# Performance work log

Hardware: AMD Instinct MI355X
Metric: run time of the kernel (lower is better)

## Reference

```python
import jax, jax.numpy as jnp
import numpy as np

NEG_SLOPE = 0.2

def gat_conv(x, edge_index, W, a_src, a_dst, b):
    # PyG GATConv, heads=1, eval mode (dropout off), add_self_loops=True
    N = x.shape[0]
    h = x @ W                                   # [N, C]
    loops = jnp.arange(N, dtype=edge_index.dtype)
    src = jnp.concatenate([edge_index[0], loops])
    dst = jnp.concatenate([edge_index[1], loops])
    s_src = h @ a_src                            # [N]
    s_dst = h @ a_dst                            # [N]
    e = s_src[src] + s_dst[dst]                  # [E+N]
    e = jnp.where(e > 0, e, NEG_SLOPE * e)       # leaky_relu
    # segment softmax over destination neighborhoods
    m = jax.ops.segment_max(e, dst, num_segments=N)
    ex = jnp.exp(e - m[dst])
    denom = jax.ops.segment_sum(ex, dst, num_segments=N)
    alpha = ex / denom[dst]                      # [E+N]
    out = jax.ops.segment_sum(alpha[:, None] * h[src], dst, num_segments=N)
    return out + b

def setup_inputs() -> dict:
    key = jax.random.key(0)
    ks = jax.random.split(key, 10)
    N, F_in, H, C, E = 100000, 256, 128, 40, 1600000
    x = jax.random.normal(ks[0], (N, F_in), dtype=jnp.float32)
    edge_index = jax.random.randint(ks[1], (2, E), 0, N, dtype=jnp.int64)
    s1 = 1.0 / np.sqrt(F_in)
    s2 = 1.0 / np.sqrt(H)
    W1 = jax.random.normal(ks[2], (F_in, H), dtype=jnp.float32) * s1
    a_src1 = jax.random.normal(ks[3], (H,), dtype=jnp.float32) * s2
    a_dst1 = jax.random.normal(ks[4], (H,), dtype=jnp.float32) * s2
    b1 = jnp.zeros((H,), dtype=jnp.float32)
    W2 = jax.random.normal(ks[5], (H, C), dtype=jnp.float32) * s2
    a_src2 = jax.random.normal(ks[6], (C,), dtype=jnp.float32) * 0.1
    a_dst2 = jax.random.normal(ks[7], (C,), dtype=jnp.float32) * 0.1
    b2 = jnp.zeros((C,), dtype=jnp.float32)
    return {"x": x, "edge_index": edge_index, "W1": W1, "a_src1": a_src1,
            "a_dst1": a_dst1, "b1": b1, "W2": W2, "a_src2": a_src2,
            "a_dst2": a_dst2, "b2": b2}

def reference(x, edge_index, W1, a_src1, a_dst1, b1, W2, a_src2, a_dst2, b2):
    h = gat_conv(x, edge_index, W1, a_src1, a_dst1, b1)
    h = jax.nn.relu(h)
    # dropout(p=0.6) is identity in eval mode
    h = gat_conv(h, edge_index, W2, a_src2, a_dst2, b2)
    return jax.nn.log_softmax(h, axis=1)
```

## Files before the change

### kernel.cpp

```cpp
#include <hip/hip_runtime.h>
#include <math.h>

#define NEG_SLOPE 0.2f
#define CAP 64
#define NB 64
#define NBUCKET 1563
#define BCAP 1408
#define BINCHUNK 2048
#define NBIN2 782

typedef __attribute__((ext_vector_type(8))) short short8;
typedef __attribute__((ext_vector_type(4))) short short4v;
typedef __attribute__((ext_vector_type(4))) float f32x4;
typedef __attribute__((ext_vector_type(2))) float f32x2;

__device__ inline unsigned short f2bf(float f) {
    union { float f; unsigned u; } x; x.f = f;
    unsigned r = x.u + 0x7FFFu + ((x.u >> 16) & 1u);
    return (unsigned short)(r >> 16);
}

__device__ __forceinline__ void gload_lds16(const void* g, void* l) {
    __builtin_amdgcn_global_load_lds(
        (const __attribute__((address_space(1))) void*)g,
        (__attribute__((address_space(3))) void*)l, 16, 0, 0);
}


__global__ __launch_bounds__(256) void front_kernel(
    const int* __restrict__ ei, int* __restrict__ bcnt,
    unsigned* __restrict__ bbuf, int E,
    const float* __restrict__ W1, const float* __restrict__ W2,
    short* __restrict__ bsw1, short* __restrict__ bsw2)
{
    __shared__ int lc[NBUCKET];
    const int tid = threadIdx.x;

    if (blockIdx.x < NBIN2) {
        const int base = blockIdx.x * BINCHUNK;
        int n = E - base; if (n > BINCHUNK) n = BINCHUNK;

        for (int b = tid; b < NBUCKET; b += 256) lc[b] = 0;
        __syncthreads();
        for (int i = tid; i < n; i += 256)
            atomicAdd(&lc[ei[E + base + i] >> 6], 1);
        __syncthreads();
        for (int b = tid; b < NBUCKET; b += 256) {
            int c = lc[b];
            lc[b] = c ? atomicAdd(&bcnt[b], c) : 0;
        }
        __syncthreads();
        for (int i = tid; i < n; i += 256) {
            int s = ei[base + i];
            int d = ei[E + base + i];
            int b = d >> 6;
            int pos = atomicAdd(&lc[b], 1);
            if (pos < BCAP)
                bbuf[(size_t)b * BCAP + pos] = (unsigned)s | ((unsigned)(d & 63) << 17);
        }
    } else {
        int t = (blockIdx.x - NBIN2) * 256 + tid;
        if (t < 4096) {
            int lane = t & 63;
            int f = t >> 6;
            int k_step = f & 7;
            int n_tile = f >> 3;
            int n  = n_tile * 16 + (lane & 15);
            int k0 = k_step * 32 + (lane >> 4) * 8;
            short8 v;
            #pragma unroll
            for (int j = 0; j < 8; j++)
                v[j] = (short)f2bf(W1[(size_t)(k0 + j) * 128 + n]);
            ((short8*)bsw1)[t] = v;
        } else if (t < 4096 + 768) {
            int u = t - 4096;
            int lane = u & 63;
            int f = u >> 6;
            int k_step = f & 3;
            int n_tile = f >> 2;
            int n  = n_tile * 16 + (lane & 15);
            int k0 = k_step * 32 + (lane >> 4) * 8;
            short8 v;
            #pragma unroll
            for (int j = 0; j < 8; j++)
                v[j] = (n < 40) ? (short)f2bf(W2[(size_t)(k0 + j) * 40 + n]) : (short)0;
            ((short8*)bsw2)[u] = v;
        }
    }
}

__global__ __launch_bounds__(256, 2) void mid_kernel(
    const int* __restrict__ bcnt, const unsigned* __restrict__ bbuf,
    int* __restrict__ csr, int* __restrict__ sorted, int* __restrict__ clsCnt,
    const float* __restrict__ x, const short* __restrict__ bsw,
    const float* __restrict__ a_src, const float* __restrict__ a_dst,
    unsigned char* __restrict__ h1, float* __restrict__ s_src,
    float* __restrict__ s_dst, int M)
{
    __shared__ __align__(16) char smem[16896];
    const int tid = threadIdx.x;
    const int bi = blockIdx.x;
    const int vb = bi >> 1;

    if ((bi & 1) == 0) {
        int* lcnt = (int*)smem;
        int (*lcsr)[CAP] = (int(*)[CAP])(smem + 256);
        int* chist = (int*)(smem + 256 + 16384);
        int* cbase = (int*)(smem + 256 + 16384 + 16);

        const int b = vb;
        const int nb = b * NB;

        if (tid < NB) lcnt[tid] = 0;
        if (tid < 4) chist[tid] = 0;
        __syncthreads();

        if (tid < NB && nb + tid < M) {
            int pos = atomicAdd(&lcnt[tid], 1);
            if (pos < CAP) lcsr[tid][pos] = nb + tid;
        }

        int ne = bcnt[b]; if (ne > BCAP) ne = BCAP;
        const unsigned* __restrict__ bp = bbuf + (size_t)b * BCAP;
        for (int j = tid; j < ne; j += 256) {
            unsigned v = bp[j];
            int s  = v & 0x1FFFF;
            int dl = v >> 17;
            int pos = atomicAdd(&lcnt[dl], 1);
            if (pos < CAP) lcsr[dl][pos] = s;
        }
        __syncthreads();

        const int4* __restrict__ srcp = (const int4*)&lcsr[0][0];
        int4* __restrict__ dstp = (int4*)(csr + (size_t)nb * CAP);
        #pragma unroll 4
        for (int j = tid; j < NB * CAP / 4; j += 256) dstp[j] = srcp[j];

        int deg = 0, cls = 0, pos = 0;
        bool isNode = (tid < NB && nb + tid < M);
        if (isNode) {
            deg = lcnt[tid]; if (deg > CAP) deg = CAP;
            cls = (deg - 1) >> 4;
            pos = atomicAdd(&chist[cls], 1);
        }
        __syncthreads();
        if (tid < 4) cbase[tid] = chist[tid] ? atomicAdd(&clsCnt[tid], chist[tid]) : 0;
        __syncthreads();
        if (isNode)
            sorted[(size_t)cls * M + cbase[cls] + pos] = (nb + tid) | (deg << 17);
        return;
    }

    const int wave = tid >> 6, lane = tid & 63;
    short8* lbs = (short8*)smem;
    const int rowBase = vb * 64;
    const int arow = rowBase + wave * 16 + (lane & 15);
    const int acol0 = (lane >> 4) * 8;
    const bool rv = (arow < M);
    const float* __restrict__ xr = x + (size_t)arow * 256 + acol0;
    const char* __restrict__ bsb = (const char*)bsw;

    auto stage = [&](int buf, int nt) {
        const char* s = bsb + nt * 8192 + wave * 2048 + lane * 16;
        char* d = smem + buf * 8192 + wave * 2048 + lane * 16;
        gload_lds16(s, d);
        gload_lds16(s + 1024, d + 1024);
    };

    stage(0, 0);

    float4 px[8], qx[8];
    #pragma unroll
    for (int k = 0; k < 8; k++) {
        px[k] = make_float4(0.f, 0.f, 0.f, 0.f);
        qx[k] = px[k];
        if (rv) {
            px[k] = *(const float4*)(xr + k * 32);
            qx[k] = *(const float4*)(xr + k * 32 + 4);
        }
    }
    short8 a[8];
    #pragma unroll
    for (int k = 0; k < 8; k++) {
        short8 t;
        t[0] = (short)f2bf(px[k].x); t[1] = (short)f2bf(px[k].y);
        t[2] = (short)f2bf(px[k].z); t[3] = (short)f2bf(px[k].w);
        t[4] = (short)f2bf(qx[k].x); t[5] = (short)f2bf(qx[k].y);
        t[6] = (short)f2bf(qx[k].z); t[7] = (short)f2bf(qx[k].w);
        a[k] = t;
    }

    const int R0 = rowBase + wave * 16 + (lane >> 4) * 4;
    const int Cb = lane & 15;

    float asv[8], adv[8];
    #pragma unroll
    for (int nt = 0; nt < 8; nt++) {
        asv[nt] = a_src[nt * 16 + Cb];
        adv[nt] = a_dst[nt * 16 + Cb];
    }

    stage(1, 1);

    float ss[4] = {0.f, 0.f, 0.f, 0.f};
    float sd[4] = {0.f, 0.f, 0.f, 0.f};
    f32x4 prev = {0.f, 0.f, 0.f, 0.f};
    int wpk[4][4];

    #pragma unroll
    for (int nt = 0; nt < 8; nt++) {
        if (nt == 7) asm volatile("s_waitcnt vmcnt(0)" ::: "memory");
        else         asm volatile("s_waitcnt vmcnt(2)" ::: "memory");
        __builtin_amdgcn_s_barrier();

        short8 breg[8];
        #pragma unroll
        for (int k = 0; k < 8; k++) breg[k] = lbs[(nt & 1) * 512 + k * 64 + lane];
        asm volatile("s_waitcnt lgkmcnt(0)" ::: "memory");
        __builtin_amdgcn_sched_barrier(0);
        __builtin_amdgcn_s_barrier();

        if (nt < 6) stage(nt & 1, nt + 2);

        __builtin_amdgcn_s_setprio(1);
        f32x4 acc = {0.f, 0.f, 0.f, 0.f};
        #pragma unroll
        for (int k = 0; k < 8; k++)
            acc = __builtin_amdgcn_mfma_f32_16x16x32_bf16(a[k], breg[k], acc, 0, 0, 0);
        __builtin_amdgcn_s_setprio(0);

        float as_ = asv[nt], ad_ = adv[nt];
        #pragma unroll
        for (int r = 0; r < 4; r++) {
            float v = acc[r];
            ss[r] = fmaf(v, as_, ss[r]);
            sd[r] = fmaf(v, ad_, sd[r]);
        }
        if (nt & 1) {
            #pragma unroll
            for (int r = 0; r < 4; r++)
                wpk[nt >> 1][r] = __builtin_amdgcn_cvt_pk_fp8_f32(prev[r], acc[r], 0, false);
        } else {
            prev = acc;
        }
    }

    #pragma unroll
    for (int r = 0; r < 4; r++) {
        int R = R0 + r;
        if (R < M) {
            #pragma unroll
            for (int t = 0; t < 4; t++)
                *(unsigned short*)(h1 + (size_t)R * 128 + t * 32 + 2 * Cb) =
                    (unsigned short)wpk[t][r];
        }
    }
    #pragma unroll
    for (int off = 1; off < 16; off <<= 1) {
        #pragma unroll
        for (int r = 0; r < 4; r++) {
            ss[r] += __shfl_xor(ss[r], off);
            sd[r] += __shfl_xor(sd[r], off);
        }
    }
    if ((lane & 15) == 0) {
        #pragma unroll
        for (int r = 0; r < 4; r++) {
            int R = R0 + r;
            if (R < M) { s_src[R] = ss[r]; s_dst[R] = sd[r]; }
        }
    }
}

__global__ __launch_bounds__(256, 4) void agg1_kernel(
    const unsigned char* __restrict__ h, const int* __restrict__ csr,
    const int* __restrict__ sorted, const int* __restrict__ clsCnt,
    const float* __restrict__ s_src, const float* __restrict__ s_dst,
    const float* __restrict__ bias,
    const short* __restrict__ bsw2,
    const float* __restrict__ a_src2, const float* __restrict__ a_dst2,
    unsigned char* __restrict__ h2, float* __restrict__ ss2,
    float* __restrict__ sd2, int N)
{
    __shared__ short lrow[16][136];
    __shared__ int   lnode[16];
    const int tid = threadIdx.x;
    const int lane = tid & 63;
    const int c = lane & 15;
    const int base = lane & 48;
    const int grp = tid >> 4;
    const int g = blockIdx.x * 16 + grp;

    int c0 = clsCnt[0], c01 = c0 + clsCnt[1], c012 = c01 + clsCnt[2];
    int cls, local;
    if (g < c0)        { cls = 0; local = g; }
    else if (g < c01)  { cls = 1; local = g - c0; }
    else if (g < c012) { cls = 2; local = g - c01; }
    else               { cls = 3; local = g - c012; }

    int ent = sorted[(size_t)cls * N + local];
    int n = ent & 0x1FFFF;
    int deg = ent >> 17;
    const int* __restrict__ edges = csr + (size_t)n * CAP;
    float sdn = s_dst[n];

    int s0 = 0, s1 = 0, s2 = 0, s3 = 0;
    float e0 = -1e30f, e1 = -1e30f, e2 = -1e30f, e3 = -1e30f;
    if (c < deg)      { s0 = edges[c];      e0 = s_src[s0] + sdn; }
    if (c + 16 < deg) { s1 = edges[c + 16]; e1 = s_src[s1] + sdn; }
    if (c + 32 < deg) { s2 = edges[c + 32]; e2 = s_src[s2] + sdn; }
    if (c + 48 < deg) { s3 = edges[c + 48]; e3 = s_src[s3] + sdn; }
    e0 = e0 > 0.f ? e0 : NEG_SLOPE * e0;
    e1 = e1 > 0.f ? e1 : NEG_SLOPE * e1;
    e2 = e2 > 0.f ? e2 : NEG_SLOPE * e2;
    e3 = e3 > 0.f ? e3 : NEG_SLOPE * e3;
    float m = fmaxf(fmaxf(e0, e1), fmaxf(e2, e3));
    #pragma unroll
    for (int off = 1; off < 16; off <<= 1) m = fmaxf(m, __shfl_xor(m, off));
    float w0 = (c < deg)      ? __expf(e0 - m) : 0.f;
    float w1 = (c + 16 < deg) ? __expf(e1 - m) : 0.f;
    float w2 = (c + 32 < deg) ? __expf(e2 - m) : 0.f;
    float w3 = (c + 48 < deg) ? __expf(e3 - m) : 0.f;
    float denom = (w0 + w1) + (w2 + w3);
    #pragma unroll
    for (int off = 1; off < 16; off <<= 1) denom += __shfl_xor(denom, off);
    float inv = 1.0f / denom;

    const uint2* __restrict__ hp = (const uint2*)h;
    f32x2 acc0 = {0.f, 0.f}, acc1 = {0.f, 0.f}, acc2 = {0.f, 0.f}, acc3 = {0.f, 0.f};

#define AGG1_BLK(K, SK, WK)                                                  \
    if (16 * K < deg) {                                                      \
        uint2 u[16];                                                         \
        _Pragma("unroll")                                                    \
        for (int jj = 0; jj < 16; jj++) {                                    \
            int sv = __shfl(SK, base + jj);                                  \
            u[jj] = hp[(size_t)sv * 16 + c];                                 \
        }                                                                    \
        _Pragma("unroll")                                                    \
        for (int jj = 0; jj < 16; jj++) {                                    \
            float wv = __shfl(WK, base + jj);                                \
            f32x2 p;                                                         \
            p = __builtin_amdgcn_cvt_pk_f32_fp8(u[jj].x, false); acc0 += p * wv; \
            p = __builtin_amdgcn_cvt_pk_f32_fp8(u[jj].x, true);  acc1 += p * wv; \
            p = __builtin_amdgcn_cvt_pk_f32_fp8(u[jj].y, false); acc2 += p * wv; \
            p = __builtin_amdgcn_cvt_pk_f32_fp8(u[jj].y, true);  acc3 += p * wv; \
        }                                                                    \
    }
    AGG1_BLK(0, s0, w0)
    AGG1_BLK(1, s1, w1)
    AGG1_BLK(2, s2, w2)
    AGG1_BLK(3, s3, w3)
#undef AGG1_BLK

    int cA = 32 * (c >> 2) + 4 * (c & 3);
    float4 bA = *(const float4*)&bias[cA];
    float4 bB = *(const float4*)&bias[cA + 16];
    float r0 = fmaxf(fmaf(acc0.x, inv, bA.x), 0.f);
    float r1 = fmaxf(fmaf(acc1.x, inv, bA.y), 0.f);
    float r2 = fmaxf(fmaf(acc2.x, inv, bA.z), 0.f);
    float r3 = fmaxf(fmaf(acc3.x, inv, bA.w), 0.f);
    float q0 = fmaxf(fmaf(acc0.y, inv, bB.x), 0.f);
    float q1 = fmaxf(fmaf(acc1.y, inv, bB.y), 0.f);
    float q2 = fmaxf(fmaf(acc2.y, inv, bB.z), 0.f);
    float q3 = fmaxf(fmaf(acc3.y, inv, bB.w), 0.f);
    short4v oA = { (short)f2bf(r0), (short)f2bf(r1), (short)f2bf(r2), (short)f2bf(r3) };
    short4v oB = { (short)f2bf(q0), (short)f2bf(q1), (short)f2bf(q2), (short)f2bf(q3) };
    *(short4v*)&lrow[grp][cA] = oA;
    *(short4v*)&lrow[grp][cA + 16] = oB;
    if (c == 0) lnode[grp] = n;
    __syncthreads();

    if (tid >= 64) return;

    const short8* __restrict__ bs = (const short8*)bsw2;
    short8 a[4];
    #pragma unroll
    for (int k = 0; k < 4; k++)
        a[k] = *(const short8*)&lrow[lane & 15][(lane >> 4) * 8 + k * 32];

    float accs[3][4];
    float ssv[4] = {0.f, 0.f, 0.f, 0.f};
    float sdv[4] = {0.f, 0.f, 0.f, 0.f};

    #pragma unroll
    for (int nt = 0; nt < 3; nt++) {
        f32x4 acc = {0.f, 0.f, 0.f, 0.f};
        #pragma unroll
        for (int k = 0; k < 4; k++) {
            short8 b = bs[(nt * 4 + k) * 64 + lane];
            acc = __builtin_amdgcn_mfma_f32_16x16x32_bf16(a[k], b, acc, 0, 0, 0);
        }
        int C = nt * 16 + c;
        bool valid = (C < 40);
        float as_ = valid ? a_src2[C] : 0.f;
        float ad_ = valid ? a_dst2[C] : 0.f;
        #pragma unroll
        for (int r = 0; r < 4; r++) {
            float v = acc[r];
            accs[nt][r] = v;
            ssv[r] = fmaf(v, as_, ssv[r]);
            sdv[r] = fmaf(v, ad_, sdv[r]);
        }
    }
    #pragma unroll
    for (int r = 0; r < 4; r++) {
        int node = lnode[(lane >> 4) * 4 + r];
        int wA = __builtin_amdgcn_cvt_pk_fp8_f32(accs[0][r], accs[1][r], 0, false);
        int wB = __builtin_amdgcn_cvt_pk_fp8_f32(accs[2][r], 0.f, 0, false);
        *(unsigned short*)(h2 + (size_t)node * 64 + 2 * c) = (unsigned short)wA;
        *(unsigned short*)(h2 + (size_t)node * 64 + 32 + 2 * c) = (unsigned short)wB;
    }
    #pragma unroll
    for (int off = 1; off < 16; off <<= 1) {
        #pragma unroll
        for (int r = 0; r < 4; r++) {
            ssv[r] += __shfl_xor(ssv[r], off);
            sdv[r] += __shfl_xor(sdv[r], off);
        }
    }
    if (c == 0) {
        #pragma unroll
        for (int r = 0; r < 4; r++) {
            int node = lnode[(lane >> 4) * 4 + r];
            ss2[node] = ssv[r];
            sd2[node] = sdv[r];
        }
    }
}

__global__ __launch_bounds__(256, 4) void agg2_kernel(
    const unsigned char* __restrict__ h, const int* __restrict__ csr,
    const int* __restrict__ sorted, const int* __restrict__ clsCnt,
    const float* __restrict__ s_src, const float* __restrict__ s_dst,
    const float* __restrict__ bias, float* __restrict__ out, int N)
{
    const int lane = threadIdx.x & 63;
    const int c = lane & 15;
    const int base = lane & 48;
    const int g = blockIdx.x * 16 + (threadIdx.x >> 4);

    int c0 = clsCnt[0], c01 = c0 + clsCnt[1], c012 = c01 + clsCnt[2];
    int cls, local;
    if (g < c0)        { cls = 0; local = g; }
    else if (g < c01)  { cls = 1; local = g - c0; }
    else if (g < c012) { cls = 2; local = g - c01; }
    else               { cls = 3; local = g - c012; }

    int ent = sorted[(size_t)cls * N + local];
    int n = ent & 0x1FFFF;
    int deg = ent >> 17;
    const int* __restrict__ edges = csr + (size_t)n * CAP;
    float sdn = s_dst[n];

    int s0 = 0, s1 = 0, s2 = 0, s3 = 0;
    float e0 = -1e30f, e1 = -1e30f, e2 = -1e30f, e3 = -1e30f;
    if (c < deg)      { s0 = edges[c];      e0 = s_src[s0] + sdn; }
    if (c + 16 < deg) { s1 = edges[c + 16]; e1 = s_src[s1] + sdn; }
    if (c + 32 < deg) { s2 = edges[c + 32]; e2 = s_src[s2] + sdn; }
    if (c + 48 < deg) { s3 = edges[c + 48]; e3 = s_src[s3] + sdn; }
    e0 = e0 > 0.f ? e0 : NEG_SLOPE * e0;
    e1 = e1 > 0.f ? e1 : NEG_SLOPE * e1;
    e2 = e2 > 0.f ? e2 : NEG_SLOPE * e2;
    e3 = e3 > 0.f ? e3 : NEG_SLOPE * e3;
    float m = fmaxf(fmaxf(e0, e1), fmaxf(e2, e3));
    #pragma unroll
    for (int off = 1; off < 16; off <<= 1) m = fmaxf(m, __shfl_xor(m, off));
    float w0 = (c < deg)      ? __expf(e0 - m) : 0.f;
    float w1 = (c + 16 < deg) ? __expf(e1 - m) : 0.f;
    float w2 = (c + 32 < deg) ? __expf(e2 - m) : 0.f;
    float w3 = (c + 48 < deg) ? __expf(e3 - m) : 0.f;
    float denom = (w0 + w1) + (w2 + w3);
    #pragma unroll
    for (int off = 1; off < 16; off <<= 1) denom += __shfl_xor(denom, off);
    float inv = 1.0f / denom;

    const unsigned* __restrict__ hp = (const unsigned*)h;
    f32x2 acc0 = {0.f, 0.f}, acc1 = {0.f, 0.f};

#define AGG2_BLK(K, SK, WK)                                                  \
    if (16 * K < deg) {                                                      \
        unsigned u[16];                                                      \
        _Pragma("unroll")                                                    \
        for (int jj = 0; jj < 16; jj++) {                                    \
            int sv = __shfl(SK, base + jj);                                  \
            u[jj] = hp[(size_t)sv * 16 + c];                                 \
        }                                                                    \
        _Pragma("unroll")                                                    \
        for (int jj = 0; jj < 16; jj++) {                                    \
            float wv = __shfl(WK, base + jj);                                \
            f32x2 p;                                                         \
            p = __builtin_amdgcn_cvt_pk_f32_fp8(u[jj], false); acc0 += p * wv; \
            p = __builtin_amdgcn_cvt_pk_f32_fp8(u[jj], true);  acc1 += p * wv; \
        }                                                                    \
    }
    AGG2_BLK(0, s0, w0)
    AGG2_BLK(1, s1, w1)
    AGG2_BLK(2, s2, w2)
    AGG2_BLK(3, s3, w3)
#undef AGG2_BLK

    float v0 = -1e30f, v1 = -1e30f, v2 = -1e30f, v3 = -1e30f;
    bool has01 = (c < 8), has0 = (c < 12);
    if (has01) {
        v0 = fmaf(acc0.x, inv, bias[2*c]);
        v1 = fmaf(acc0.y, inv, bias[2*c + 16]);
        v2 = fmaf(acc1.x, inv, bias[2*c + 1]);
        v3 = fmaf(acc1.y, inv, bias[2*c + 17]);
    } else if (has0) {
        v0 = fmaf(acc0.x, inv, bias[2*c + 16]);
        v2 = fmaf(acc1.x, inv, bias[2*c + 17]);
    }

    float mx = fmaxf(fmaxf(v0, v1), fmaxf(v2, v3));
    #pragma unroll
    for (int off = 1; off < 16; off <<= 1) mx = fmaxf(mx, __shfl_xor(mx, off));
    float sum = 0.f;
    if (has01) sum = __expf(v0 - mx) + __expf(v1 - mx) + __expf(v2 - mx) + __expf(v3 - mx);
    else if (has0) sum = __expf(v0 - mx) + __expf(v2 - mx);
    #pragma unroll
    for (int off = 1; off < 16; off <<= 1) sum += __shfl_xor(sum, off);
    float lg = mx + __logf(sum);

    if (has01) {
        *(float2*)&out[(size_t)n * 40 + 2*c]      = make_float2(v0 - lg, v2 - lg);
        *(float2*)&out[(size_t)n * 40 + 2*c + 16] = make_float2(v1 - lg, v3 - lg);
    } else if (has0) {
        *(float2*)&out[(size_t)n * 40 + 2*c + 16] = make_float2(v0 - lg, v2 - lg);
    }
}

extern "C" void kernel_launch(void* const* d_in, const int* in_sizes, int n_in,
                              void* d_out, int out_size, void* d_ws, size_t ws_size,
                              hipStream_t stream)
{
    const float* x      = (const float*)d_in[0];
    const int*   ei     = (const int*)d_in[1];
    const float* W1     = (const float*)d_in[2];
    const float* a_src1 = (const float*)d_in[3];
    const float* a_dst1 = (const float*)d_in[4];
    const float* b1     = (const float*)d_in[5];
    const float* W2     = (const float*)d_in[6];
    const float* a_src2 = (const float*)d_in[7];
    const float* a_dst2 = (const float*)d_in[8];
    const float* b2     = (const float*)d_in[9];
    float* out = (float*)d_out;

    const int N = 100000;
    const int E = 1600000;

    char* ws = (char*)d_ws;
    size_t off = 0;
    auto alloc = [&](size_t bytes) -> void* {
        void* p = ws + off;
        off += (bytes + 255) & ~(size_t)255;
        return p;
    };
    unsigned char*  h1b  = (unsigned char*)alloc((size_t)N * 128);
    unsigned char*  h2b  = (unsigned char*)alloc((size_t)N * 64);
    int*   csr    = (int*)alloc((size_t)NBUCKET * NB * CAP * 4);
    int*   sorted = (int*)alloc((size_t)4 * N * 4);
    float* ss1  = (float*)alloc((size_t)N * 4);
    float* sd1  = (float*)alloc((size_t)N * 4);
    float* ss2  = (float*)alloc((size_t)N * 4);
    float* sd2  = (float*)alloc((size_t)N * 4);
    short* bsw1 = (short*)alloc((size_t)4096 * 8 * 2);
    short* bsw2 = (short*)alloc((size_t)768 * 8 * 2);
    int*   bcnt = (int*)alloc((size_t)(NBUCKET + 4) * 4);
    int*   clsCnt = bcnt + NBUCKET;
    unsigned* bbuf = (unsigned*)alloc((size_t)NBUCKET * BCAP * 4);

    hipMemsetAsync(bcnt, 0, (size_t)(NBUCKET + 4) * 4, stream);

    front_kernel<<<dim3(NBIN2 + 19), dim3(256), 0, stream>>>(
        ei, bcnt, bbuf, E, W1, W2, bsw1, bsw2);

    mid_kernel<<<dim3(2 * NBUCKET), dim3(256), 0, stream>>>(
        bcnt, bbuf, csr, sorted, clsCnt,
        x, bsw1, a_src1, a_dst1, h1b, ss1, sd1, N);

    agg1_kernel<<<dim3(N / 16), dim3(256), 0, stream>>>(
        h1b, csr, sorted, clsCnt, ss1, sd1, b1,
        bsw2, a_src2, a_dst2, h2b, ss2, sd2, N);

    agg2_kernel<<<dim3(N / 16), dim3(256), 0, stream>>>(
        h2b, csr, sorted, clsCnt, ss2, sd2, b2, out, N);
}
```

Measured before the change: 324.5 us.

## Build CSR by direct global-atomic scatter instead of two-level bucket sort

```diff
diff --git a/kernel.cpp b/kernel.cpp
--- a/kernel.cpp
+++ b/kernel.cpp
@@ -3,11 +3,9 @@
 
 #define NEG_SLOPE 0.2f
 #define CAP 64
-#define NB 64
-#define NBUCKET 1563
-#define BCAP 1408
-#define BINCHUNK 2048
-#define NBIN2 782
+#define SBLK 782
+#define TT 200000
+#define NCLSBLK 391
 
 typedef __attribute__((ext_vector_type(8))) short short8;
 typedef __attribute__((ext_vector_type(4))) short short4v;
@@ -27,39 +25,29 @@
 }
 
 
-__global__ __launch_bounds__(256) void front_kernel(
-    const int* __restrict__ ei, int* __restrict__ bcnt,
-    unsigned* __restrict__ bbuf, int E,
+__global__ __launch_bounds__(256) void scatter_kernel(
+    const int* __restrict__ ei, int* __restrict__ cnt,
+    int* __restrict__ csr, int E,
     const float* __restrict__ W1, const float* __restrict__ W2,
     short* __restrict__ bsw1, short* __restrict__ bsw2)
 {
-    __shared__ int lc[NBUCKET];
     const int tid = threadIdx.x;
-
-    if (blockIdx.x < NBIN2) {
-        const int base = blockIdx.x * BINCHUNK;
-        int n = E - base; if (n > BINCHUNK) n = BINCHUNK;
-
-        for (int b = tid; b < NBUCKET; b += 256) lc[b] = 0;
-        __syncthreads();
-        for (int i = tid; i < n; i += 256)
-            atomicAdd(&lc[ei[E + base + i] >> 6], 1);
-        __syncthreads();
-        for (int b = tid; b < NBUCKET; b += 256) {
-            int c = lc[b];
-            lc[b] = c ? atomicAdd(&bcnt[b], c) : 0;
-        }
-        __syncthreads();
-        for (int i = tid; i < n; i += 256) {
-            int s = ei[base + i];
-            int d = ei[E + base + i];
-            int b = d >> 6;
-            int pos = atomicAdd(&lc[b], 1);
-            if (pos < BCAP)
-                bbuf[(size_t)b * BCAP + pos] = (unsigned)s | ((unsigned)(d & 63) << 17);
-        }
+    if (blockIdx.x < SBLK) {
+        int g = blockIdx.x * 256 + tid;
+        if (g >= TT) return;
+        int s[8], d[8], pos[8];
+        #pragma unroll
+        for (int i = 0; i < 8; i++) {
+            s[i] = ei[i * TT + g];
+            d[i] = ei[E + i * TT + g];
+        }
+        #pragma unroll
+        for (int i = 0; i < 8; i++) pos[i] = atomicAdd(&cnt[d[i]], 1);
+        #pragma unroll
+        for (int i = 0; i < 8; i++)
+            if (pos[i] < CAP - 1) csr[(size_t)d[i] * CAP + pos[i]] = s[i];
     } else {
-        int t = (blockIdx.x - NBIN2) * 256 + tid;
+        int t = (blockIdx.x - SBLK) * 256 + tid;
         if (t < 4096) {
             int lane = t & 63;
             int f = t >> 6;
@@ -90,8 +78,8 @@
 }
 
 __global__ __launch_bounds__(256, 2) void mid_kernel(
-    const int* __restrict__ bcnt, const unsigned* __restrict__ bbuf,
-    int* __restrict__ csr, int* __restrict__ sorted, int* __restrict__ clsCnt,
+    const int* __restrict__ cnt, int* __restrict__ sorted,
+    int* __restrict__ clsCnt,
     const float* __restrict__ x, const short* __restrict__ bsw,
     const float* __restrict__ a_src, const float* __restrict__ a_dst,
     unsigned char* __restrict__ h1, float* __restrict__ s_src,
@@ -99,61 +87,32 @@
 {
     __shared__ __align__(16) char smem[16896];
     const int tid = threadIdx.x;
-    const int bi = blockIdx.x;
-    const int vb = bi >> 1;
-
-    if ((bi & 1) == 0) {
-        int* lcnt = (int*)smem;
-        int (*lcsr)[CAP] = (int(*)[CAP])(smem + 256);
-        int* chist = (int*)(smem + 256 + 16384);
-        int* cbase = (int*)(smem + 256 + 16384 + 16);
-
-        const int b = vb;
-        const int nb = b * NB;
-
-        if (tid < NB) lcnt[tid] = 0;
+
+    if (blockIdx.x < NCLSBLK) {
+        int* chist = (int*)smem;
+        int* cbase = (int*)(smem + 16);
+        int n = blockIdx.x * 256 + tid;
+        bool v = (n < M);
         if (tid < 4) chist[tid] = 0;
         __syncthreads();
-
-        if (tid < NB && nb + tid < M) {
-            int pos = atomicAdd(&lcnt[tid], 1);
-            if (pos < CAP) lcsr[tid][pos] = nb + tid;
-        }
-
-        int ne = bcnt[b]; if (ne > BCAP) ne = BCAP;
-        const unsigned* __restrict__ bp = bbuf + (size_t)b * BCAP;
-        for (int j = tid; j < ne; j += 256) {
-            unsigned v = bp[j];
-            int s  = v & 0x1FFFF;
-            int dl = v >> 17;
-            int pos = atomicAdd(&lcnt[dl], 1);
-            if (pos < CAP) lcsr[dl][pos] = s;
-        }
-        __syncthreads();
-
-        const int4* __restrict__ srcp = (const int4*)&lcsr[0][0];
-        int4* __restrict__ dstp = (int4*)(csr + (size_t)nb * CAP);
-        #pragma unroll 4
-        for (int j = tid; j < NB * CAP / 4; j += 256) dstp[j] = srcp[j];
-
-        int deg = 0, cls = 0, pos = 0;
-        bool isNode = (tid < NB && nb + tid < M);
-        if (isNode) {
-            deg = lcnt[tid]; if (deg > CAP) deg = CAP;
-            cls = (deg - 1) >> 4;
+        int degt = 0, cls = 0, pos = 0;
+        if (v) {
+            int dn = cnt[n]; if (dn > CAP - 1) dn = CAP - 1;
+            degt = dn + 1;
+            cls = (degt - 1) >> 4;
             pos = atomicAdd(&chist[cls], 1);
         }
         __syncthreads();
         if (tid < 4) cbase[tid] = chist[tid] ? atomicAdd(&clsCnt[tid], chist[tid]) : 0;
         __syncthreads();
-        if (isNode)
-            sorted[(size_t)cls * M + cbase[cls] + pos] = (nb + tid) | (deg << 17);
+        if (v)
+            sorted[(size_t)cls * M + cbase[cls] + pos] = n | (degt << 17);
         return;
     }
 
     const int wave = tid >> 6, lane = tid & 63;
     short8* lbs = (short8*)smem;
-    const int rowBase = vb * 64;
+    const int rowBase = (blockIdx.x - NCLSBLK) * 64;
     const int arow = rowBase + wave * 16 + (lane & 15);
     const int acol0 = (lane >> 4) * 8;
     const bool rv = (arow < M);
@@ -300,16 +259,17 @@
 
     int ent = sorted[(size_t)cls * N + local];
     int n = ent & 0x1FFFF;
-    int deg = ent >> 17;
+    int degt = ent >> 17;
+    int dn = degt - 1;
     const int* __restrict__ edges = csr + (size_t)n * CAP;
     float sdn = s_dst[n];
 
     int s0 = 0, s1 = 0, s2 = 0, s3 = 0;
     float e0 = -1e30f, e1 = -1e30f, e2 = -1e30f, e3 = -1e30f;
-    if (c < deg)      { s0 = edges[c];      e0 = s_src[s0] + sdn; }
-    if (c + 16 < deg) { s1 = edges[c + 16]; e1 = s_src[s1] + sdn; }
-    if (c + 32 < deg) { s2 = edges[c + 32]; e2 = s_src[s2] + sdn; }
-    if (c + 48 < deg) { s3 = edges[c + 48]; e3 = s_src[s3] + sdn; }
+    if (c < degt)      { s0 = (c < dn)      ? edges[c]      : n; e0 = s_src[s0] + sdn; }
+    if (c + 16 < degt) { s1 = (c + 16 < dn) ? edges[c + 16] : n; e1 = s_src[s1] + sdn; }
+    if (c + 32 < degt) { s2 = (c + 32 < dn) ? edges[c + 32] : n; e2 = s_src[s2] + sdn; }
+    if (c + 48 < degt) { s3 = (c + 48 < dn) ? edges[c + 48] : n; e3 = s_src[s3] + sdn; }
     e0 = e0 > 0.f ? e0 : NEG_SLOPE * e0;
     e1 = e1 > 0.f ? e1 : NEG_SLOPE * e1;
     e2 = e2 > 0.f ? e2 : NEG_SLOPE * e2;
@@ -317,10 +277,10 @@
     float m = fmaxf(fmaxf(e0, e1), fmaxf(e2, e3));
     #pragma unroll
     for (int off = 1; off < 16; off <<= 1) m = fmaxf(m, __shfl_xor(m, off));
-    float w0 = (c < deg)      ? __expf(e0 - m) : 0.f;
-    float w1 = (c + 16 < deg) ? __expf(e1 - m) : 0.f;
-    float w2 = (c + 32 < deg) ? __expf(e2 - m) : 0.f;
-    float w3 = (c + 48 < deg) ? __expf(e3 - m) : 0.f;
+    float w0 = (c < degt)      ? __expf(e0 - m) : 0.f;
+    float w1 = (c + 16 < degt) ? __expf(e1 - m) : 0.f;
+    float w2 = (c + 32 < degt) ? __expf(e2 - m) : 0.f;
+    float w3 = (c + 48 < degt) ? __expf(e3 - m) : 0.f;
     float denom = (w0 + w1) + (w2 + w3);
     #pragma unroll
     for (int off = 1; off < 16; off <<= 1) denom += __shfl_xor(denom, off);
@@ -330,7 +290,7 @@
     f32x2 acc0 = {0.f, 0.f}, acc1 = {0.f, 0.f}, acc2 = {0.f, 0.f}, acc3 = {0.f, 0.f};
 
 #define AGG1_BLK(K, SK, WK)                                                  \
-    if (16 * K < deg) {                                                      \
+    if (16 * K < degt) {                                                     \
         uint2 u[16];                                                         \
         _Pragma("unroll")                                                    \
         for (int jj = 0; jj < 16; jj++) {                                    \
@@ -449,16 +409,17 @@
 
     int ent = sorted[(size_t)cls * N + local];
     int n = ent & 0x1FFFF;
-    int deg = ent >> 17;
+    int degt = ent >> 17;
+    int dn = degt - 1;
     const int* __restrict__ edges = csr + (size_t)n * CAP;
     float sdn = s_dst[n];
 
     int s0 = 0, s1 = 0, s2 = 0, s3 = 0;
     float e0 = -1e30f, e1 = -1e30f, e2 = -1e30f, e3 = -1e30f;
-    if (c < deg)      { s0 = edges[c];      e0 = s_src[s0] + sdn; }
-    if (c + 16 < deg) { s1 = edges[c + 16]; e1 = s_src[s1] + sdn; }
-    if (c + 32 < deg) { s2 = edges[c + 32]; e2 = s_src[s2] + sdn; }
-    if (c + 48 < deg) { s3 = edges[c + 48]; e3 = s_src[s3] + sdn; }
+    if (c < degt)      { s0 = (c < dn)      ? edges[c]      : n; e0 = s_src[s0] + sdn; }
+    if (c + 16 < degt) { s1 = (c + 16 < dn) ? edges[c + 16] : n; e1 = s_src[s1] + sdn; }
+    if (c + 32 < degt) { s2 = (c + 32 < dn) ? edges[c + 32] : n; e2 = s_src[s2] + sdn; }
+    if (c + 48 < degt) { s3 = (c + 48 < dn) ? edges[c + 48] : n; e3 = s_src[s3] + sdn; }
     e0 = e0 > 0.f ? e0 : NEG_SLOPE * e0;
     e1 = e1 > 0.f ? e1 : NEG_SLOPE * e1;
     e2 = e2 > 0.f ? e2 : NEG_SLOPE * e2;
@@ -466,10 +427,10 @@
     float m = fmaxf(fmaxf(e0, e1), fmaxf(e2, e3));
     #pragma unroll
     for (int off = 1; off < 16; off <<= 1) m = fmaxf(m, __shfl_xor(m, off));
-    float w0 = (c < deg)      ? __expf(e0 - m) : 0.f;
-    float w1 = (c + 16 < deg) ? __expf(e1 - m) : 0.f;
-    float w2 = (c + 32 < deg) ? __expf(e2 - m) : 0.f;
-    float w3 = (c + 48 < deg) ? __expf(e3 - m) : 0.f;
+    float w0 = (c < degt)      ? __expf(e0 - m) : 0.f;
+    float w1 = (c + 16 < degt) ? __expf(e1 - m) : 0.f;
+    float w2 = (c + 32 < degt) ? __expf(e2 - m) : 0.f;
+    float w3 = (c + 48 < degt) ? __expf(e3 - m) : 0.f;
     float denom = (w0 + w1) + (w2 + w3);
     #pragma unroll
     for (int off = 1; off < 16; off <<= 1) denom += __shfl_xor(denom, off);
@@ -479,7 +440,7 @@
     f32x2 acc0 = {0.f, 0.f}, acc1 = {0.f, 0.f};
 
 #define AGG2_BLK(K, SK, WK)                                                  \
-    if (16 * K < deg) {                                                      \
+    if (16 * K < degt) {                                                     \
         unsigned u[16];                                                      \
         _Pragma("unroll")                                                    \
         for (int jj = 0; jj < 16; jj++) {                                    \
@@ -558,7 +519,7 @@
     };
     unsigned char*  h1b  = (unsigned char*)alloc((size_t)N * 128);
     unsigned char*  h2b  = (unsigned char*)alloc((size_t)N * 64);
-    int*   csr    = (int*)alloc((size_t)NBUCKET * NB * CAP * 4);
+    int*   csr    = (int*)alloc((size_t)N * CAP * 4);
     int*   sorted = (int*)alloc((size_t)4 * N * 4);
     float* ss1  = (float*)alloc((size_t)N * 4);
     float* sd1  = (float*)alloc((size_t)N * 4);
@@ -566,17 +527,16 @@
     float* sd2  = (float*)alloc((size_t)N * 4);
     short* bsw1 = (short*)alloc((size_t)4096 * 8 * 2);
     short* bsw2 = (short*)alloc((size_t)768 * 8 * 2);
-    int*   bcnt = (int*)alloc((size_t)(NBUCKET + 4) * 4);
-    int*   clsCnt = bcnt + NBUCKET;
-    unsigned* bbuf = (unsigned*)alloc((size_t)NBUCKET * BCAP * 4);
-
-    hipMemsetAsync(bcnt, 0, (size_t)(NBUCKET + 4) * 4, stream);
-
-    front_kernel<<<dim3(NBIN2 + 19), dim3(256), 0, stream>>>(
-        ei, bcnt, bbuf, E, W1, W2, bsw1, bsw2);
-
-    mid_kernel<<<dim3(2 * NBUCKET), dim3(256), 0, stream>>>(
-        bcnt, bbuf, csr, sorted, clsCnt,
+    int*   cnt  = (int*)alloc((size_t)(N + 4) * 4);
+    int*   clsCnt = cnt + N;
+
+    hipMemsetAsync(cnt, 0, (size_t)(N + 4) * 4, stream);
+
+    scatter_kernel<<<dim3(SBLK + 19), dim3(256), 0, stream>>>(
+        ei, cnt, csr, E, W1, W2, bsw1, bsw2);
+
+    mid_kernel<<<dim3(NCLSBLK + (N + 63) / 64), dim3(256), 0, stream>>>(
+        cnt, sorted, clsCnt,
         x, bsw1, a_src1, a_dst1, h1b, ss1, sd1, N);
 
     agg1_kernel<<<dim3(N / 16), dim3(256), 0, stream>>>(
```

New measurement: 383.7 us. 18.2% more time.

## Overlap edge binning with layer-1 GEMM and split CSR fill into own kernel

Applied to the files above, without the earlier changes.

```diff
diff --git a/kernel.cpp b/kernel.cpp
--- a/kernel.cpp
+++ b/kernel.cpp
@@ -6,8 +6,8 @@
 #define NB 64
 #define NBUCKET 1563
 #define BCAP 1408
-#define BINCHUNK 2048
-#define NBIN2 782
+#define BINCHUNK 8192
+#define NBINB 196
 
 typedef __attribute__((ext_vector_type(8))) short short8;
 typedef __attribute__((ext_vector_type(4))) short short4v;
@@ -27,17 +27,59 @@
 }
 
 
-__global__ __launch_bounds__(256) void front_kernel(
+__global__ __launch_bounds__(256) void init_kernel(
+    const float* __restrict__ W1, const float* __restrict__ W2,
+    short* __restrict__ bsw1, short* __restrict__ bsw2,
+    int* __restrict__ ctrl)
+{
+    int t = blockIdx.x * 256 + threadIdx.x;
+    if (t < 4096) {
+        int lane = t & 63;
+        int f = t >> 6;
+        int k_step = f & 7;
+        int n_tile = f >> 3;
+        int n  = n_tile * 16 + (lane & 15);
+        int k0 = k_step * 32 + (lane >> 4) * 8;
+        short8 v;
+        #pragma unroll
+        for (int j = 0; j < 8; j++)
+            v[j] = (short)f2bf(W1[(size_t)(k0 + j) * 128 + n]);
+        ((short8*)bsw1)[t] = v;
+    } else if (t < 4096 + 768) {
+        int u = t - 4096;
+        int lane = u & 63;
+        int f = u >> 6;
+        int k_step = f & 3;
+        int n_tile = f >> 2;
+        int n  = n_tile * 16 + (lane & 15);
+        int k0 = k_step * 32 + (lane >> 4) * 8;
+        short8 v;
+        #pragma unroll
+        for (int j = 0; j < 8; j++)
+            v[j] = (n < 40) ? (short)f2bf(W2[(size_t)(k0 + j) * 40 + n]) : (short)0;
+        ((short8*)bsw2)[u] = v;
+    } else {
+        for (int i = t - 4864; i < NBUCKET + 4; i += 256)
+            if (i >= 0) ctrl[i] = 0;
+    }
+}
+
+__global__ __launch_bounds__(256, 2) void k1_kernel(
     const int* __restrict__ ei, int* __restrict__ bcnt,
     unsigned* __restrict__ bbuf, int E,
-    const float* __restrict__ W1, const float* __restrict__ W2,
-    short* __restrict__ bsw1, short* __restrict__ bsw2)
+    const float* __restrict__ x, const short* __restrict__ bsw,
+    const float* __restrict__ a_src, const float* __restrict__ a_dst,
+    unsigned char* __restrict__ h1, float* __restrict__ s_src,
+    float* __restrict__ s_dst, int M)
 {
-    __shared__ int lc[NBUCKET];
+    __shared__ __align__(16) char smem[16896];
     const int tid = threadIdx.x;
-
-    if (blockIdx.x < NBIN2) {
-        const int base = blockIdx.x * BINCHUNK;
+    const int bi = blockIdx.x;
+    const int q = bi / 9, r = bi - q * 9;
+
+    if (r == 0 && q < NBINB) {
+        int* lc = (int*)smem;
+        const int base = q * BINCHUNK;
         int n = E - base; if (n > BINCHUNK) n = BINCHUNK;
 
         for (int b = tid; b < NBUCKET; b += 256) lc[b] = 0;
@@ -58,99 +100,11 @@
             if (pos < BCAP)
                 bbuf[(size_t)b * BCAP + pos] = (unsigned)s | ((unsigned)(d & 63) << 17);
         }
-    } else {
-        int t = (blockIdx.x - NBIN2) * 256 + tid;
-        if (t < 4096) {
-            int lane = t & 63;
-            int f = t >> 6;
-            int k_step = f & 7;
-            int n_tile = f >> 3;
-            int n  = n_tile * 16 + (lane & 15);
-            int k0 = k_step * 32 + (lane >> 4) * 8;
-            short8 v;
-            #pragma unroll
-            for (int j = 0; j < 8; j++)
-                v[j] = (short)f2bf(W1[(size_t)(k0 + j) * 128 + n]);
-            ((short8*)bsw1)[t] = v;
-        } else if (t < 4096 + 768) {
-            int u = t - 4096;
-            int lane = u & 63;
-            int f = u >> 6;
-            int k_step = f & 3;
-            int n_tile = f >> 2;
-            int n  = n_tile * 16 + (lane & 15);
-            int k0 = k_step * 32 + (lane >> 4) * 8;
-            short8 v;
-            #pragma unroll
-            for (int j = 0; j < 8; j++)
-                v[j] = (n < 40) ? (short)f2bf(W2[(size_t)(k0 + j) * 40 + n]) : (short)0;
-            ((short8*)bsw2)[u] = v;
-        }
-    }
-}
-
-__global__ __launch_bounds__(256, 2) void mid_kernel(
-    const int* __restrict__ bcnt, const unsigned* __restrict__ bbuf,
-    int* __restrict__ csr, int* __restrict__ sorted, int* __restrict__ clsCnt,
-    const float* __restrict__ x, const short* __restrict__ bsw,
-    const float* __restrict__ a_src, const float* __restrict__ a_dst,
-    unsigned char* __restrict__ h1, float* __restrict__ s_src,
-    float* __restrict__ s_dst, int M)
-{
-    __shared__ __align__(16) char smem[16896];
-    const int tid = threadIdx.x;
-    const int bi = blockIdx.x;
-    const int vb = bi >> 1;
-
-    if ((bi & 1) == 0) {
-        int* lcnt = (int*)smem;
-        int (*lcsr)[CAP] = (int(*)[CAP])(smem + 256);
-        int* chist = (int*)(smem + 256 + 16384);
-        int* cbase = (int*)(smem + 256 + 16384 + 16);
-
-        const int b = vb;
-        const int nb = b * NB;
-
-        if (tid < NB) lcnt[tid] = 0;
-        if (tid < 4) chist[tid] = 0;
-        __syncthreads();
-
-        if (tid < NB && nb + tid < M) {
-            int pos = atomicAdd(&lcnt[tid], 1);
-            if (pos < CAP) lcsr[tid][pos] = nb + tid;
-        }
-
-        int ne = bcnt[b]; if (ne > BCAP) ne = BCAP;
-        const unsigned* __restrict__ bp = bbuf + (size_t)b * BCAP;
-        for (int j = tid; j < ne; j += 256) {
-            unsigned v = bp[j];
-            int s  = v & 0x1FFFF;
-            int dl = v >> 17;
-            int pos = atomicAdd(&lcnt[dl], 1);
-            if (pos < CAP) lcsr[dl][pos] = s;
-        }
-        __syncthreads();
-
-        const int4* __restrict__ srcp = (const int4*)&lcsr[0][0];
-        int4* __restrict__ dstp = (int4*)(csr + (size_t)nb * CAP);
-        #pragma unroll 4
-        for (int j = tid; j < NB * CAP / 4; j += 256) dstp[j] = srcp[j];
-
-        int deg = 0, cls = 0, pos = 0;
-        bool isNode = (tid < NB && nb + tid < M);
-        if (isNode) {
-            deg = lcnt[tid]; if (deg > CAP) deg = CAP;
-            cls = (deg - 1) >> 4;
-            pos = atomicAdd(&chist[cls], 1);
-        }
-        __syncthreads();
-        if (tid < 4) cbase[tid] = chist[tid] ? atomicAdd(&clsCnt[tid], chist[tid]) : 0;
-        __syncthreads();
-        if (isNode)
-            sorted[(size_t)cls * M + cbase[cls] + pos] = (nb + tid) | (deg << 17);
         return;
     }
 
+    const int nbin = (q < NBINB) ? (q + (r ? 1 : 0)) : NBINB;
+    const int vb = bi - nbin;
     const int wave = tid >> 6, lane = tid & 63;
     short8* lbs = (short8*)smem;
     const int rowBase = vb * 64;
@@ -231,45 +185,97 @@
 
         float as_ = asv[nt], ad_ = adv[nt];
         #pragma unroll
-        for (int r = 0; r < 4; r++) {
-            float v = acc[r];
-            ss[r] = fmaf(v, as_, ss[r]);
-            sd[r] = fmaf(v, ad_, sd[r]);
+        for (int r2 = 0; r2 < 4; r2++) {
+            float v = acc[r2];
+            ss[r2] = fmaf(v, as_, ss[r2]);
+            sd[r2] = fmaf(v, ad_, sd[r2]);
         }
         if (nt & 1) {
             #pragma unroll
-            for (int r = 0; r < 4; r++)
-                wpk[nt >> 1][r] = __builtin_amdgcn_cvt_pk_fp8_f32(prev[r], acc[r], 0, false);
+            for (int r2 = 0; r2 < 4; r2++)
+                wpk[nt >> 1][r2] = __builtin_amdgcn_cvt_pk_fp8_f32(prev[r2], acc[r2], 0, false);
         } else {
             prev = acc;
         }
     }
 
     #pragma unroll
-    for (int r = 0; r < 4; r++) {
-        int R = R0 + r;
+    for (int r2 = 0; r2 < 4; r2++) {
+        int R = R0 + r2;
         if (R < M) {
             #pragma unroll
             for (int t = 0; t < 4; t++)
                 *(unsigned short*)(h1 + (size_t)R * 128 + t * 32 + 2 * Cb) =
-                    (unsigned short)wpk[t][r];
+                    (unsigned short)wpk[t][r2];
         }
     }
     #pragma unroll
     for (int off = 1; off < 16; off <<= 1) {
         #pragma unroll
-        for (int r = 0; r < 4; r++) {
-            ss[r] += __shfl_xor(ss[r], off);
-            sd[r] += __shfl_xor(sd[r], off);
+        for (int r2 = 0; r2 < 4; r2++) {
+            ss[r2] += __shfl_xor(ss[r2], off);
+            sd[r2] += __shfl_xor(sd[r2], off);
         }
     }
     if ((lane & 15) == 0) {
         #pragma unroll
-        for (int r = 0; r < 4; r++) {
-            int R = R0 + r;
-            if (R < M) { s_src[R] = ss[r]; s_dst[R] = sd[r]; }
-        }
-    }
+        for (int r2 = 0; r2 < 4; r2++) {
+            int R = R0 + r2;
+            if (R < M) { s_src[R] = ss[r2]; s_dst[R] = sd[r2]; }
+        }
+    }
+}
+
+__global__ __launch_bounds__(256) void fill_kernel(
+    const int* __restrict__ bcnt, const unsigned* __restrict__ bbuf,
+    int* __restrict__ csr, int* __restrict__ sorted, int* __restrict__ clsCnt,
+    int M)
+{
+    __shared__ int lcnt[NB];
+    __shared__ int lcsr[NB][CAP];
+    __shared__ int chist[4];
+    __shared__ int cbase[4];
+    const int tid = threadIdx.x;
+    const int b = blockIdx.x;
+    const int nb = b * NB;
+
+    if (tid < NB) lcnt[tid] = 0;
+    if (tid < 4) chist[tid] = 0;
+    __syncthreads();
+
+    if (tid < NB && nb + tid < M) {
+        int pos = atomicAdd(&lcnt[tid], 1);
+        if (pos < CAP) lcsr[tid][pos] = nb + tid;
+    }
+
+    int ne = bcnt[b]; if (ne > BCAP) ne = BCAP;
+    const unsigned* __restrict__ bp = bbuf + (size_t)b * BCAP;
+    for (int j = tid; j < ne; j += 256) {
+        unsigned v = bp[j];
+        int s  = v & 0x1FFFF;
+        int dl = v >> 17;
+        int pos = atomicAdd(&lcnt[dl], 1);
+        if (pos < CAP) lcsr[dl][pos] = s;
+    }
+    __syncthreads();
+
+    const int4* __restrict__ srcp = (const int4*)&lcsr[0][0];
+    int4* __restrict__ dstp = (int4*)(csr + (size_t)nb * CAP);
+    #pragma unroll 4
+    for (int j = tid; j < NB * CAP / 4; j += 256) dstp[j] = srcp[j];
+
+    int deg = 0, cls = 0, pos = 0;
+    bool isNode = (tid < NB && nb + tid < M);
+    if (isNode) {
+        deg = lcnt[tid]; if (deg > CAP) deg = CAP;
+        cls = (deg - 1) >> 4;
+        pos = atomicAdd(&chist[cls], 1);
+    }
+    __syncthreads();
+    if (tid < 4) cbase[tid] = chist[tid] ? atomicAdd(&clsCnt[tid], chist[tid]) : 0;
+    __syncthreads();
+    if (isNode)
+        sorted[(size_t)cls * M + cbase[cls] + pos] = (nb + tid) | (deg << 17);
 }
 
 __global__ __launch_bounds__(256, 4) void agg1_kernel(
@@ -566,18 +572,19 @@
     float* sd2  = (float*)alloc((size_t)N * 4);
     short* bsw1 = (short*)alloc((size_t)4096 * 8 * 2);
     short* bsw2 = (short*)alloc((size_t)768 * 8 * 2);
-    int*   bcnt = (int*)alloc((size_t)(NBUCKET + 4) * 4);
-    int*   clsCnt = bcnt + NBUCKET;
+    int*   ctrl = (int*)alloc((size_t)(NBUCKET + 4) * 4);
+    int*   bcnt   = ctrl;
+    int*   clsCnt = ctrl + NBUCKET;
     unsigned* bbuf = (unsigned*)alloc((size_t)NBUCKET * BCAP * 4);
 
-    hipMemsetAsync(bcnt, 0, (size_t)(NBUCKET + 4) * 4, stream);
-
-    front_kernel<<<dim3(NBIN2 + 19), dim3(256), 0, stream>>>(
-        ei, bcnt, bbuf, E, W1, W2, bsw1, bsw2);
-
-    mid_kernel<<<dim3(2 * NBUCKET), dim3(256), 0, stream>>>(
-        bcnt, bbuf, csr, sorted, clsCnt,
+    init_kernel<<<dim3(20), dim3(256), 0, stream>>>(W1, W2, bsw1, bsw2, ctrl);
+
+    k1_kernel<<<dim3(NBINB + (N + 63) / 64), dim3(256), 0, stream>>>(
+        ei, bcnt, bbuf, E,
         x, bsw1, a_src1, a_dst1, h1b, ss1, sd1, N);
+
+    fill_kernel<<<dim3(NBUCKET), dim3(256), 0, stream>>>(
+        bcnt, bbuf, csr, sorted, clsCnt, N);
 
     agg1_kernel<<<dim3(N / 16), dim3(256), 0, stream>>>(
         h1b, csr, sorted, clsCnt, ss1, sd1, b1,
```

New measurement: 340.6 us. 5.0% more time.
